# Kernel tuning notes

Hardware: AMD Instinct MI355X
Metric: run time of the kernel (lower is better)

The kernel has to match this reference:

```python
import jax, jax.numpy as jnp
import numpy as np

T_TEST, B, F, H, N_OUT = 8192, 8, 100, 512, 1


def setup_inputs() -> dict:
    key = jax.random.key(0)
    ks = jax.random.split(key, 7)
    s = 0.05  # keep generated-weight magnitudes in a realistic hypernetwork range
    return {
        "x_test": jax.random.normal(ks[0], (T_TEST, B, F), dtype=jnp.float32),
        "w1": jax.random.normal(ks[1], (B, F, H), dtype=jnp.float32) * s,
        "b1": jax.random.normal(ks[2], (B, H), dtype=jnp.float32) * s,
        "w2": jax.random.normal(ks[3], (B, H, H), dtype=jnp.float32) * s,
        "b2": jax.random.normal(ks[4], (B, H), dtype=jnp.float32) * s,
        "w3": jax.random.normal(ks[5], (B, H, N_OUT), dtype=jnp.float32) * s,
        "b3": jax.random.normal(ks[6], (B, N_OUT), dtype=jnp.float32) * s,
    }


def reference(x_test, w1, b1, w2, b2, w3, b3):
    # MotherNet.nn_forward with predicted_activation='relu',
    # weight_embedding_rank=None, low_rank_last=False.
    # Original torch: h = (x.unsqueeze(-1) * w.unsqueeze(0)).sum(2) + b
    # == per-dataset batched GEMM over the B axis.
    x = jnp.nan_to_num(x_test)                    # [T, B, F]
    h = jnp.einsum('tbf,bfh->tbh', x, w1) + b1    # [T, B, H]
    h = jax.nn.relu(h)
    h = jnp.einsum('tbf,bfh->tbh', h, w2) + b2    # [T, B, H]
    h = jax.nn.relu(h)
    h = jnp.einsum('tbf,bfh->tbh', h, w3) + b3    # [T, B, 1]
    return h
```

## Files before the change

kernel.cpp:

```cpp
#include <hip/hip_runtime.h>

#define T_TEST 8192
#define BB 8
#define FF 100
#define HH 512

typedef __bf16 bf16x8 __attribute__((ext_vector_type(8)));
typedef float f32x16 __attribute__((ext_vector_type(16)));
typedef unsigned short u16;
typedef unsigned int u32;

__device__ __forceinline__ u16 f2bf(float f) {
    u32 u = __float_as_uint(f);
    u += 0x7fffu + ((u >> 16) & 1);
    return (u16)(u >> 16);
}

__device__ __forceinline__ float nan2num(float v) {
    u32 u = __float_as_uint(v);
    if ((u & 0x7f800000u) == 0x7f800000u) {
        v = (u & 0x007fffffu) ? 0.f : ((u >> 31) ? -3.3895314e38f : 3.3895314e38f);
    }
    return v;
}

__global__ void prep_w(const float* __restrict__ w1, const float* __restrict__ w2,
                       u16* __restrict__ w1f, u16* __restrict__ w2f) {
    int bid = blockIdx.x;
    if (bid < 256) {
        int t = bid * 256 + threadIdx.x;
        int lane = t & 63;
        int n32 = (t >> 6) & 15;
        int b = t >> 13;
        int n = n32 * 32 + (lane & 31);
        int kb = ((t >> 10) & 7) * 16 + (lane >> 5) * 8;
        u32 p[4];
#pragma unroll
        for (int jp = 0; jp < 4; ++jp) {
            int k0 = kb + jp * 2;
            float v0 = (k0 < FF)     ? w1[(b * FF + k0) * HH + n]     : 0.f;
            float v1 = (k0 + 1 < FF) ? w1[(b * FF + k0 + 1) * HH + n] : 0.f;
            p[jp] = (u32)f2bf(v0) | ((u32)f2bf(v1) << 16);
        }
        uint4 o = {p[0], p[1], p[2], p[3]};
        *(uint4*)(w1f + (size_t)t * 8) = o;
    } else {
        int t = (bid - 256) * 256 + threadIdx.x;
        int lane = t & 63;
        int n32 = (t >> 6) & 15;
        int b = t >> 15;
        int n = n32 * 32 + (lane & 31);
        int kb = ((t >> 10) & 31) * 16 + (lane >> 5) * 8;
        u32 p[4];
#pragma unroll
        for (int jp = 0; jp < 4; ++jp) {
            int k0 = kb + jp * 2;
            float v0 = w2[(b * HH + k0) * HH + n];
            float v1 = w2[(b * HH + k0 + 1) * HH + n];
            p[jp] = (u32)f2bf(v0) | ((u32)f2bf(v1) << 16);
        }
        uint4 o = {p[0], p[1], p[2], p[3]};
        *(uint4*)(w2f + (size_t)t * 8) = o;
    }
}

__global__ __launch_bounds__(512, 2) void l1_kernel(
    const float* __restrict__ x, const u16* __restrict__ w1f,
    const float* __restrict__ b1, u16* __restrict__ h1g) {
    __shared__ __align__(16) char lds[81920];
    u16* xf  = (u16*)lds;
    u16* h1f = (u16*)(lds + 16384);

    const int tid = threadIdx.x;
    const int b = blockIdx.x;
    const int m0 = blockIdx.y * 64;
    const int lane = tid & 63;
    const int ws = __builtin_amdgcn_readfirstlane(tid >> 6);
    const int l31 = lane & 31, lh = lane >> 5;
    const int n32b = ws * 2;

    const bf16x8* W1 = (const bf16x8*)w1f + (size_t)b * 8192;

    bf16x8 pa[2][2], pb[4][2];

#pragma unroll
    for (int s = 0; s < 4; ++s)
#pragma unroll
        for (int ni = 0; ni < 2; ++ni)
            pb[s][ni] = W1[(s * 16 + n32b + ni) * 64 + lane];

    float b1v[2];
    b1v[0] = b1[b * HH + (n32b + 0) * 32 + l31];
    b1v[1] = b1[b * HH + (n32b + 1) * 32 + l31];

    if (ws < 7) {
        int row = lane, s = ws;
        int mi = row >> 5, m = row & 31;
        const float* xr = x + ((size_t)(m0 + row) * BB + b) * FF + s * 16;
        u32 p[8];
#pragma unroll
        for (int i = 0; i < 8; ++i) p[i] = 0;
        if (s <= 5) {
#pragma unroll
            for (int j = 0; j < 4; ++j) {
                float4 v = *(const float4*)(xr + j * 4);
                p[j * 2 + 0] = (u32)f2bf(nan2num(v.x)) | ((u32)f2bf(nan2num(v.y)) << 16);
                p[j * 2 + 1] = (u32)f2bf(nan2num(v.z)) | ((u32)f2bf(nan2num(v.w)) << 16);
            }
        } else {
            float4 v = *(const float4*)(xr);
            p[0] = (u32)f2bf(nan2num(v.x)) | ((u32)f2bf(nan2num(v.y)) << 16);
            p[1] = (u32)f2bf(nan2num(v.z)) | ((u32)f2bf(nan2num(v.w)) << 16);
        }
        int fi1 = s * 2 + mi;
        uint4 g0 = {p[0], p[1], p[2], p[3]};
        uint4 g1 = {p[4], p[5], p[6], p[7]};
        *(uint4*)(xf + (fi1 * 64 + m) * 8)      = g0;
        *(uint4*)(xf + (fi1 * 64 + 32 + m) * 8) = g1;
    }
    __syncthreads();

    f32x16 acc1[2][2] = {};
#pragma unroll
    for (int s = 0; s < 2; ++s)
#pragma unroll
        for (int mi = 0; mi < 2; ++mi)
            pa[s][mi] = *(const bf16x8*)(xf + ((s * 2 + mi) * 64 + lane) * 8);
#pragma unroll
    for (int ks = 0; ks < 7; ++ks) {
        const int pA = ks & 1, pB = ks & 3;
        bf16x8 a0 = pa[pA][0], a1 = pa[pA][1];
        bf16x8 b0 = pb[pB][0], b1r = pb[pB][1];
        if (ks < 5) {
#pragma unroll
            for (int mi = 0; mi < 2; ++mi)
                pa[pA][mi] = *(const bf16x8*)(xf + (((ks + 2) * 2 + mi) * 64 + lane) * 8);
        }
        if (ks < 3) {
#pragma unroll
            for (int ni = 0; ni < 2; ++ni)
                pb[pB][ni] = W1[((ks + 4) * 16 + n32b + ni) * 64 + lane];
        }
        acc1[0][0] = __builtin_amdgcn_mfma_f32_32x32x16_bf16(a0, b0,  acc1[0][0], 0, 0, 0);
        acc1[0][1] = __builtin_amdgcn_mfma_f32_32x32x16_bf16(a0, b1r, acc1[0][1], 0, 0, 0);
        acc1[1][0] = __builtin_amdgcn_mfma_f32_32x32x16_bf16(a1, b0,  acc1[1][0], 0, 0, 0);
        acc1[1][1] = __builtin_amdgcn_mfma_f32_32x32x16_bf16(a1, b1r, acc1[1][1], 0, 0, 0);
    }

    {
        char* hw = (char*)h1f + (l31 >> 4) * 2048 + ((l31 >> 3) & 1) * 512 +
                   (l31 & 6) * 2 + lh * 64 + n32b * 4096;
#pragma unroll
        for (int ni = 0; ni < 2; ++ni) {
#pragma unroll
            for (int mi = 0; mi < 2; ++mi)
#pragma unroll
                for (int qd = 0; qd < 4; ++qd) {
                    u32 own01 = (u32)f2bf(fmaxf(acc1[mi][ni][qd * 4 + 0] + b1v[ni], 0.f)) |
                                ((u32)f2bf(fmaxf(acc1[mi][ni][qd * 4 + 1] + b1v[ni], 0.f)) << 16);
                    u32 own23 = (u32)f2bf(fmaxf(acc1[mi][ni][qd * 4 + 2] + b1v[ni], 0.f)) |
                                ((u32)f2bf(fmaxf(acc1[mi][ni][qd * 4 + 3] + b1v[ni], 0.f)) << 16);
                    u32 oth01 = __shfl_xor(own01, 1, 64);
                    u32 oth23 = __shfl_xor(own23, 1, 64);
                    char* base = hw + ni * 4096 + mi * 1024 + qd * 128;
                    if (!(lane & 1)) {
                        *(u32*)(base +  0) = (own01 & 0xffffu) | (oth01 << 16);
                        *(u32*)(base + 16) = (own01 >> 16) | (oth01 & 0xffff0000u);
                    } else {
                        *(u32*)(base + 32) = (oth23 & 0xffffu) | (own23 << 16);
                        *(u32*)(base + 48) = (oth23 >> 16) | (own23 & 0xffff0000u);
                    }
                }
        }
    }
    __syncthreads();

    {
        const uint4* src = (const uint4*)h1f;
        uint4* dst = (uint4*)(h1g + (size_t)(b * 128 + blockIdx.y) * 32768);
#pragma unroll
        for (int j = 0; j < 8; ++j)
            dst[tid + j * 512] = src[tid + j * 512];
    }
}

__global__ __launch_bounds__(512, 4) void l23_kernel(
    const u16* __restrict__ h1g, const u16* __restrict__ w2f,
    const float* __restrict__ b2, const float* __restrict__ w3,
    const float* __restrict__ b3, float* __restrict__ out) {
    __shared__ float part[512];

    const int tid = threadIdx.x;
    const int b = blockIdx.x;
    const int m0 = blockIdx.y * 64;
    const int lane = tid & 63;
    const int ws = __builtin_amdgcn_readfirstlane(tid >> 6);
    const int l31 = lane & 31, lh = lane >> 5;
    const int n32b = ws * 2;

    const bf16x8* W2 = (const bf16x8*)w2f + (size_t)b * 32768;
    const char* Ab = (const char*)(h1g + (size_t)(b * 128 + blockIdx.y) * 32768) +
                     (size_t)lane * 16;

    bf16x8 pa[2][2], pb[4][2];

#pragma unroll
    for (int s = 0; s < 4; ++s)
#pragma unroll
        for (int ni = 0; ni < 2; ++ni)
            pb[s][ni] = W2[(s * 16 + n32b + ni) * 64 + lane];

    float b2v[2], w3v[2];
#pragma unroll
    for (int ni = 0; ni < 2; ++ni) {
        int n = (n32b + ni) * 32 + l31;
        b2v[ni] = b2[b * HH + n];
        w3v[ni] = w3[b * HH + n];
    }

#pragma unroll
    for (int s = 0; s < 2; ++s)
#pragma unroll
        for (int mi = 0; mi < 2; ++mi)
            pa[s][mi] = *(const bf16x8*)(Ab + (s * 2 + mi) * 1024);

    f32x16 acc2[2][2] = {};
#pragma unroll
    for (int ks = 0; ks < 32; ++ks) {
        const int pA = ks & 1, pB = ks & 3;
        bf16x8 a0 = pa[pA][0], a1 = pa[pA][1];
        bf16x8 b0 = pb[pB][0], b1r = pb[pB][1];
        if (ks < 30) {
#pragma unroll
            for (int mi = 0; mi < 2; ++mi)
                pa[pA][mi] = *(const bf16x8*)(Ab + ((ks + 2) * 2 + mi) * 1024);
        }
        if (ks < 28) {
#pragma unroll
            for (int ni = 0; ni < 2; ++ni)
                pb[pB][ni] = W2[((ks + 4) * 16 + n32b + ni) * 64 + lane];
        }
        acc2[0][0] = __builtin_amdgcn_mfma_f32_32x32x16_bf16(a0, b0,  acc2[0][0], 0, 0, 0);
        acc2[0][1] = __builtin_amdgcn_mfma_f32_32x32x16_bf16(a0, b1r, acc2[0][1], 0, 0, 0);
        acc2[1][0] = __builtin_amdgcn_mfma_f32_32x32x16_bf16(a1, b0,  acc2[1][0], 0, 0, 0);
        acc2[1][1] = __builtin_amdgcn_mfma_f32_32x32x16_bf16(a1, b1r, acc2[1][1], 0, 0, 0);
    }

#pragma unroll
    for (int mi = 0; mi < 2; ++mi)
#pragma unroll
        for (int r = 0; r < 16; ++r) {
            float v = fmaxf(acc2[mi][0][r] + b2v[0], 0.f) * w3v[0] +
                      fmaxf(acc2[mi][1][r] + b2v[1], 0.f) * w3v[1];
            v += __shfl_xor(v, 1, 64);
            v += __shfl_xor(v, 2, 64);
            v += __shfl_xor(v, 4, 64);
            v += __shfl_xor(v, 8, 64);
            v += __shfl_xor(v, 16, 64);
            if (l31 == 0)
                part[ws * 64 + mi * 32 + (r & 3) + 8 * (r >> 2) + 4 * lh] = v;
        }
    __syncthreads();
    if (tid < 64) {
        float s = b3[b];
#pragma unroll
        for (int ww = 0; ww < 8; ++ww) s += part[ww * 64 + tid];
        out[(size_t)(m0 + tid) * BB + b] = s;
    }
}

extern "C" void kernel_launch(void* const* d_in, const int* in_sizes, int n_in,
                              void* d_out, int out_size, void* d_ws, size_t ws_size,
                              hipStream_t stream) {
    const float* x  = (const float*)d_in[0];
    const float* w1 = (const float*)d_in[1];
    const float* b1 = (const float*)d_in[2];
    const float* w2 = (const float*)d_in[3];
    const float* b2 = (const float*)d_in[4];
    const float* w3 = (const float*)d_in[5];
    const float* b3 = (const float*)d_in[6];
    float* out = (float*)d_out;

    u16* w1f = (u16*)d_ws;
    u16* w2f = w1f + (size_t)BB * 8192 * 8;
    u16* h1g = w2f + (size_t)BB * 32768 * 8;

    prep_w<<<1280, 256, 0, stream>>>(w1, w2, w1f, w2f);
    l1_kernel<<<dim3(BB, T_TEST / 64), 512, 0, stream>>>(x, w1f, b1, h1g);
    l23_kernel<<<dim3(BB, T_TEST / 64), 512, 0, stream>>>(h1g, w2f, b2, w3, b3, out);
}
```

Measured before the change: 156.7 us.

## Stage W2 column slice in LDS and split N across blocks with atomic output

The layer-2/3 kernel is regridded so that each block owns one 64-column slice of W2 for one dataset. That slice is staged once into 64KB of LDS and reused over 1024 rows, instead of every block streaming the whole W2 from global memory. Partial results of the final layer-3 dot product are combined across column slices with atomicAdd into an output first filled with the b3 bias by a new init kernel. In exchange, each block rereads the h1 activations through 8 row tiles, relies on float atomics so summation order is nondeterministic, and uses large LDS that limits occupancy.

```diff
diff --git a/kernel.cpp b/kernel.cpp
--- a/kernel.cpp
+++ b/kernel.cpp
@@ -62,6 +62,11 @@
         uint4 o = {p[0], p[1], p[2], p[3]};
         *(uint4*)(w2f + (size_t)t * 8) = o;
     }
+}
+
+__global__ void init_out(const float* __restrict__ b3, float* __restrict__ out) {
+    int i = blockIdx.x * 256 + threadIdx.x;
+    out[i] = b3[i & 7];
 }
 
 __global__ __launch_bounds__(512, 2) void l1_kernel(
@@ -187,28 +192,30 @@
 __global__ __launch_bounds__(512, 4) void l23_kernel(
     const u16* __restrict__ h1g, const u16* __restrict__ w2f,
     const float* __restrict__ b2, const float* __restrict__ w3,
-    const float* __restrict__ b3, float* __restrict__ out) {
-    __shared__ float part[512];
+    float* __restrict__ out) {
+    __shared__ __align__(16) char ldsB[65536];
 
     const int tid = threadIdx.x;
-    const int b = blockIdx.x;
-    const int m0 = blockIdx.y * 64;
+    const int bx = blockIdx.x;
+    const int b = bx >> 3, rg = bx & 7;
+    const int nsl = blockIdx.y;
     const int lane = tid & 63;
     const int ws = __builtin_amdgcn_readfirstlane(tid >> 6);
     const int l31 = lane & 31, lh = lane >> 5;
-    const int n32b = ws * 2;
-
-    const bf16x8* W2 = (const bf16x8*)w2f + (size_t)b * 32768;
-    const char* Ab = (const char*)(h1g + (size_t)(b * 128 + blockIdx.y) * 32768) +
-                     (size_t)lane * 16;
-
-    bf16x8 pa[2][2], pb[4][2];
-
-#pragma unroll
-    for (int s = 0; s < 4; ++s)
-#pragma unroll
-        for (int ni = 0; ni < 2; ++ni)
-            pb[s][ni] = W2[(s * 16 + n32b + ni) * 64 + lane];
+    const int n32b = nsl * 2;
+
+    {
+        const char* W2b = (const char*)w2f + (size_t)b * 524288;
+#pragma unroll
+        for (int j = 0; j < 8; ++j) {
+            int g = j * 512 + tid;
+            int f = g >> 6, l = g & 63;
+            int ks = f >> 1, ni = f & 1;
+            int srcfrag = (ks * 16 + n32b + ni) * 64 + l;
+            *(uint4*)(ldsB + (size_t)g * 16) =
+                *(const uint4*)(W2b + (size_t)srcfrag * 16);
+        }
+    }
 
     float b2v[2], w3v[2];
 #pragma unroll
@@ -217,55 +224,56 @@
         b2v[ni] = b2[b * HH + n];
         w3v[ni] = w3[b * HH + n];
     }
-
-#pragma unroll
-    for (int s = 0; s < 2; ++s)
-#pragma unroll
-        for (int mi = 0; mi < 2; ++mi)
-            pa[s][mi] = *(const bf16x8*)(Ab + (s * 2 + mi) * 1024);
-
-    f32x16 acc2[2][2] = {};
-#pragma unroll
-    for (int ks = 0; ks < 32; ++ks) {
-        const int pA = ks & 1, pB = ks & 3;
-        bf16x8 a0 = pa[pA][0], a1 = pa[pA][1];
-        bf16x8 b0 = pb[pB][0], b1r = pb[pB][1];
-        if (ks < 30) {
-#pragma unroll
-            for (int mi = 0; mi < 2; ++mi)
-                pa[pA][mi] = *(const bf16x8*)(Ab + ((ks + 2) * 2 + mi) * 1024);
-        }
-        if (ks < 28) {
+    __syncthreads();
+
+#pragma unroll
+    for (int i = 0; i < 4; ++i) {
+        int rt = ws + 8 * i;
+        int tile64 = rg * 16 + (rt >> 1);
+        int mi = rt & 1;
+        const char* Ab = (const char*)h1g + (size_t)(b * 128 + tile64) * 65536 +
+                         mi * 1024 + (size_t)lane * 16;
+
+        bf16x8 pa[2], pb[2][2];
+        pa[0] = *(const bf16x8*)(Ab);
+        pa[1] = *(const bf16x8*)(Ab + 2048);
+#pragma unroll
+        for (int s = 0; s < 2; ++s)
 #pragma unroll
             for (int ni = 0; ni < 2; ++ni)
-                pb[pB][ni] = W2[((ks + 4) * 16 + n32b + ni) * 64 + lane];
-        }
-        acc2[0][0] = __builtin_amdgcn_mfma_f32_32x32x16_bf16(a0, b0,  acc2[0][0], 0, 0, 0);
-        acc2[0][1] = __builtin_amdgcn_mfma_f32_32x32x16_bf16(a0, b1r, acc2[0][1], 0, 0, 0);
-        acc2[1][0] = __builtin_amdgcn_mfma_f32_32x32x16_bf16(a1, b0,  acc2[1][0], 0, 0, 0);
-        acc2[1][1] = __builtin_amdgcn_mfma_f32_32x32x16_bf16(a1, b1r, acc2[1][1], 0, 0, 0);
-    }
-
-#pragma unroll
-    for (int mi = 0; mi < 2; ++mi)
+                pb[s][ni] = *(const bf16x8*)(ldsB + ((s * 2 + ni) * 64 + lane) * 16);
+
+        f32x16 acc[2] = {};
+#pragma unroll
+        for (int ks = 0; ks < 32; ++ks) {
+            const int p = ks & 1;
+            bf16x8 a0 = pa[p];
+            bf16x8 b0 = pb[p][0], b1r = pb[p][1];
+            if (ks < 30) {
+                pa[p] = *(const bf16x8*)(Ab + (ks + 2) * 2048);
+#pragma unroll
+                for (int ni = 0; ni < 2; ++ni)
+                    pb[p][ni] = *(const bf16x8*)(ldsB + (((ks + 2) * 2 + ni) * 64 + lane) * 16);
+            }
+            acc[0] = __builtin_amdgcn_mfma_f32_32x32x16_bf16(a0, b0,  acc[0], 0, 0, 0);
+            acc[1] = __builtin_amdgcn_mfma_f32_32x32x16_bf16(a0, b1r, acc[1], 0, 0, 0);
+        }
+
+        int rowbase = tile64 * 64 + mi * 32;
 #pragma unroll
         for (int r = 0; r < 16; ++r) {
-            float v = fmaxf(acc2[mi][0][r] + b2v[0], 0.f) * w3v[0] +
-                      fmaxf(acc2[mi][1][r] + b2v[1], 0.f) * w3v[1];
+            float v = fmaxf(acc[0][r] + b2v[0], 0.f) * w3v[0] +
+                      fmaxf(acc[1][r] + b2v[1], 0.f) * w3v[1];
             v += __shfl_xor(v, 1, 64);
             v += __shfl_xor(v, 2, 64);
             v += __shfl_xor(v, 4, 64);
             v += __shfl_xor(v, 8, 64);
             v += __shfl_xor(v, 16, 64);
-            if (l31 == 0)
-                part[ws * 64 + mi * 32 + (r & 3) + 8 * (r >> 2) + 4 * lh] = v;
-        }
-    __syncthreads();
-    if (tid < 64) {
-        float s = b3[b];
-#pragma unroll
-        for (int ww = 0; ww < 8; ++ww) s += part[ww * 64 + tid];
-        out[(size_t)(m0 + tid) * BB + b] = s;
+            if (l31 == 0) {
+                int row = rowbase + (r & 3) + 8 * (r >> 2) + 4 * lh;
+                atomicAdd(out + (size_t)row * BB + b, v);
+            }
+        }
     }
 }
 
@@ -286,6 +294,7 @@
     u16* h1g = w2f + (size_t)BB * 32768 * 8;
 
     prep_w<<<1280, 256, 0, stream>>>(w1, w2, w1f, w2f);
+    init_out<<<(T_TEST * BB) / 256, 256, 0, stream>>>(b3, out);
     l1_kernel<<<dim3(BB, T_TEST / 64), 512, 0, stream>>>(x, w1f, b1, h1g);
-    l23_kernel<<<dim3(BB, T_TEST / 64), 512, 0, stream>>>(h1g, w2f, b2, w3, b3, out);
-}
+    l23_kernel<<<dim3(64, 8), 512, 0, stream>>>(h1g, w2f, b2, w3, out);
+}
```

Result: slower. 213.5 us (+36.3%).
